# Kernel optimization log

Measured on AMD Instinct MI355X. Metric: run time of the kernel, lower is better.

## Reference

```python
import jax, jax.numpy as jnp
import numpy as np

# ---- static config (from MACEConfig / MACELayerConfig) ----
N_NODES = 128
F_S = 128          # n_invariant_feat_hidden (0e channels)
F_V = 64           # n_vectors_hidden (1e channels)
N_BESSEL = 8       # bessel_number
R_MAX = 5.0        # r_max
N_LAYERS = 2       # n_interactions
HID_RAD = 64       # radial MLP hidden width
F_S_OUT = 128      # n_invariant_feat_readout
F_V_OUT = 64       # n_vectors_readout
AVG_NEIGH = float(N_NODES)  # avg_num_neighbors default = n_nodes
RAD_OUT = F_S + 3 * F_V     # per-edge radial channel weights for the 4 TP paths


def _senders_receivers(n):
    # fully connected graph, matching get_senders_and_receivers
    s = np.repeat(np.arange(n), n - 1)
    j = np.tile(np.arange(1, n), n)
    r = (s + j) % n
    return jnp.asarray(s, dtype=jnp.int32), jnp.asarray(r, dtype=jnp.int32)


def _bessel(r):
    # e3nn bessel basis: sqrt(2/c) sin(n pi r / c) / r, n = 1..N_BESSEL
    n = jnp.arange(1, N_BESSEL + 1, dtype=r.dtype)
    return jnp.sqrt(2.0 / R_MAX) * jnp.sin(n * jnp.pi * r[:, None] / R_MAX) / r[:, None]


def _envelope(r):
    # smooth radial cutoff (polynomial p=6), stand-in for e3nn soft_envelope
    u = r / R_MAX
    p = 6.0
    env = 1.0 - (p + 1) * (p + 2) / 2 * u ** p + p * (p + 2) * u ** (p + 1) - p * (p + 1) / 2 * u ** (p + 2)
    return jnp.where(u < 1.0, env, 0.0)


def _forward(x, species_embed, Wr1, Wr2, W_sv, W_mix_s, W_mix_v, W_out_s, W_out_v):
    senders, receivers = _senders_receivers(N_NODES)

    def single(pos):  # pos: (N, 3)
        com = pos.mean(axis=0)                       # centre of mass (3,)
        v = pos[receivers] - pos[senders]            # edge relative vectors (E, 3)
        r = jnp.linalg.norm(v, axis=-1) + 1e-8       # (E,)
        vhat = v / r[:, None]
        rb = _bessel(r) * _envelope(r)[:, None]      # (E, N_BESSEL)

        s = jnp.broadcast_to(species_embed[0], (N_NODES, F_S))       # 0e node feats
        V = jnp.zeros((N_NODES, F_V, 3), dtype=pos.dtype)            # 1e node feats

        for l in range(N_LAYERS):
            # learned per-edge radial weights for each tensor-product path
            h = jax.nn.silu(rb @ Wr1[l]) @ Wr2[l]    # (E, RAD_OUT)
            R0 = h[:, :F_S]
            R1 = h[:, F_S:F_S + F_V]
            R2 = h[:, F_S + F_V:F_S + 2 * F_V]
            R3 = h[:, F_S + 2 * F_V:]

            s_src = s[senders]                       # gather (E, F_S)
            V_src = V[senders]                       # gather (E, F_V, 3)

            # CG tensor-product paths (only 0e and 1e irreps present):
            m0a = R0 * s_src                                         # 0e x 0e -> 0e
            m0b = R1 * jnp.einsum('efk,ek->ef', V_src, vhat)         # 1e x 1e -> 0e
            m1a = (R2 * (s_src @ W_sv[l]))[..., None] * vhat[:, None, :]  # 0e x 1e -> 1e
            m1b = R3[..., None] * V_src                              # 1e x 0e -> 1e

            # scatter-sum message passing over receivers
            agg0 = jax.ops.segment_sum(jnp.concatenate([m0a, m0b], -1), receivers,
                                       num_segments=N_NODES) / AVG_NEIGH   # (N, F_S+F_V)
            agg1 = jax.ops.segment_sum(jnp.concatenate([m1a, m1b], 1), receivers,
                                       num_segments=N_NODES) / AVG_NEIGH   # (N, 2F_V, 3)

            s = s + jax.nn.silu(agg0 @ W_mix_s[l])
            V = V + jnp.einsum('nfk,fg->ngk', agg1, W_mix_v[l])

        out_s = s @ W_out_s                                          # (N, F_S_OUT)
        out_v = jnp.einsum('nfk,fg->ngk', V, W_out_v) + com          # (N, F_V_OUT, 3) + CoM
        return out_v, out_s

    return jax.vmap(single)(x)


def setup_inputs() -> dict:
    key = jax.random.key(0)
    ks = jax.random.split(key, 10)
    sc = lambda fan: 1.0 / np.sqrt(fan)
    inp = {
        'x': jax.random.normal(ks[0], (8, N_NODES, 3), dtype=jnp.float32),
        'species_embed': jax.random.normal(ks[1], (1, F_S), dtype=jnp.float32),
        'Wr1': jax.random.normal(ks[2], (N_LAYERS, N_BESSEL, HID_RAD), dtype=jnp.float32) * sc(N_BESSEL),
        'Wr2': jax.random.normal(ks[3], (N_LAYERS, HID_RAD, RAD_OUT), dtype=jnp.float32) * sc(HID_RAD),
        'W_sv': jax.random.normal(ks[4], (N_LAYERS, F_S, F_V), dtype=jnp.float32) * sc(F_S),
        'W_mix_s': jax.random.normal(ks[5], (N_LAYERS, F_S + F_V, F_S), dtype=jnp.float32) * sc(F_S + F_V),
        'W_mix_v': jax.random.normal(ks[6], (N_LAYERS, 2 * F_V, F_V), dtype=jnp.float32) * sc(2 * F_V),
        'W_out_s': jax.random.normal(ks[7], (F_S, F_S_OUT), dtype=jnp.float32) * sc(F_S),
        'W_out_v': jax.random.normal(ks[8], (F_V, F_V_OUT), dtype=jnp.float32) * sc(F_V),
    }
    return inp


def reference(x, species_embed, Wr1, Wr2, W_sv, W_mix_s, W_mix_v, W_out_s, W_out_v):
    return _forward(x, species_embed, Wr1, Wr2, W_sv, W_mix_s, W_mix_v, W_out_s, W_out_v)
```

## Files before the change

kernel.cpp:

```cpp
#include <hip/hip_runtime.h>
#include <math.h>

typedef unsigned short u16;
typedef __attribute__((ext_vector_type(8))) short frag_ab;
typedef __attribute__((ext_vector_type(4))) float frag_cd;

#define BATCH 8
#define NN 128
#define FS 128
#define FV 64
#define NB 8
#define HID 64
#define ROUT 320
#define HSTRB 72

#define SZ_S (BATCH*FS*NN)
#define SZ_V (BATCH*FV*3*NN)
#define SZ_T (BATCH*FV*NN)
#define N_W2B (ROUT*HID)
#define OFF_SB 0
#define OFF_VB (OFF_SB+SZ_S)
#define OFF_T1 (OFF_VB+SZ_V)
#define OFF_W2B (OFF_T1+SZ_T)

__device__ __forceinline__ float silu_f(float x){ return x * (1.0f/(1.0f + __expf(-x))); }

__device__ __forceinline__ u16 f2bf(float x){
  union { float f; unsigned int u; } v; v.f = x;
  unsigned int r = v.u + 0x7fffu + ((v.u >> 16) & 1u);
  return (u16)(r >> 16);
}
__device__ __forceinline__ float bf2f(u16 h){
  union { unsigned int u; float f; } v; v.u = ((unsigned int)h) << 16; return v.f;
}

__global__ __launch_bounds__(512) void layer0_kernel(
    const float* __restrict__ pos,
    const float* __restrict__ species,
    const float* __restrict__ Wr1l,
    const float* __restrict__ Wr2,
    const float* __restrict__ Wsv,
    const float* __restrict__ WmixSl,
    const float* __restrict__ WmixVl,
    float* __restrict__ sOut,
    float* __restrict__ vOut,
    float* __restrict__ tOut,
    u16*   __restrict__ w2b)
{
  const int tid = threadIdx.x;
  const int b   = blockIdx.x >> 6;
  const int k0  = (blockIdx.x & 63) * 2;

  __shared__ u16   hidB[2][128*HSTRB];
  __shared__ float vhx[2][128], vhy[2][128], vhz[2][128];
  __shared__ float colsum[2][4][64];
  __shared__ float aggS[2][128];
  __shared__ float dV[2][204];
  __shared__ float sNew[2][128];
  __shared__ float t0L[64];
  __shared__ float tPart[4][2][64];

  const float* pb   = pos + b*NN*3;
  const float* Wr2l = Wr2;

  {
    const int kk   = tid >> 8;
    const int r2   = tid & 255;
    const int i    = r2 & 127;
    const int half = r2 >> 7;
    const int k    = k0 + kk;
    float vx = pb[k*3+0]-pb[i*3+0];
    float vy = pb[k*3+1]-pb[i*3+1];
    float vz = pb[k*3+2]-pb[i*3+2];
    float r = sqrtf(vx*vx+vy*vy+vz*vz) + 1e-8f;
    float inv = 1.0f/r;
    if (half==0){ vhx[kk][i]=vx*inv; vhy[kk][i]=vy*inv; vhz[kk][i]=vz*inv; }
    float u = r*0.2f;
    float env = 0.0f;
    if (u < 1.0f && i != k){
      float u2=u*u, u6=u2*u2*u2;
      env = 1.0f - 28.0f*u6 + 48.0f*u6*u - 21.0f*u6*u2;
    }
    float coef = 0.6324555320336759f * inv * env;
    float th   = r * 0.6283185307179586f;
    float s1 = __sinf(th), c1 = __cosf(th);
    float rb[NB];
    rb[0] = coef*s1;
    float twoc = 2.f*c1, sp = s1, spp = 0.f;
    #pragma unroll
    for(int n=1;n<NB;n++){ float s = twoc*sp - spp; spp = sp; sp = s; rb[n] = coef*s; }
    u16* hrow = hidB[kk] + i*HSTRB;
    #pragma unroll
    for(int jg=0;jg<8;jg++){
      const int jgg = half*8 + jg;
      float h0=0.f,h1=0.f,h2=0.f,h3=0.f;
      #pragma unroll
      for(int n=0;n<NB;n++){
        const float* wr = Wr1l + n*HID + jgg*4;
        float rn = rb[n];
        h0 = fmaf(rn, wr[0], h0);
        h1 = fmaf(rn, wr[1], h1);
        h2 = fmaf(rn, wr[2], h2);
        h3 = fmaf(rn, wr[3], h3);
      }
      ushort4 uu = make_ushort4(f2bf(silu_f(h0)), f2bf(silu_f(h1)),
                                f2bf(silu_f(h2)), f2bf(silu_f(h3)));
      *(ushort4*)(hrow + jgg*4) = uu;
    }
  }
  __syncthreads();

  if (tid < 256){
    const int kk = tid >> 7;
    const int var = (tid >> 5) & 3;
    const int jh  = tid & 31;
    const u16* hb = hidB[kk] + 2*jh;
    float a0=0.f,a1=0.f,c0_=0.f,c1_=0.f;
    if (var == 0){
      #pragma unroll 8
      for (int i=0;i<128;i+=2){
        unsigned int v0 = *(const unsigned int*)(hb + i*HSTRB);
        unsigned int v1 = *(const unsigned int*)(hb + (i+1)*HSTRB);
        a0  += bf2f((u16)(v0 & 0xffffu)); a1  += bf2f((u16)(v0 >> 16));
        c0_ += bf2f((u16)(v1 & 0xffffu)); c1_ += bf2f((u16)(v1 >> 16));
      }
    } else {
      const float* wv = (var==1) ? vhx[kk] : (var==2) ? vhy[kk] : vhz[kk];
      #pragma unroll 8
      for (int i=0;i<128;i+=2){
        unsigned int v0 = *(const unsigned int*)(hb + i*HSTRB);
        unsigned int v1 = *(const unsigned int*)(hb + (i+1)*HSTRB);
        float w0 = wv[i], w1 = wv[i+1];
        a0  = fmaf(bf2f((u16)(v0 & 0xffffu)), w0, a0);
        a1  = fmaf(bf2f((u16)(v0 >> 16)),     w0, a1);
        c0_ = fmaf(bf2f((u16)(v1 & 0xffffu)), w1, c0_);
        c1_ = fmaf(bf2f((u16)(v1 >> 16)),     w1, c1_);
      }
    }
    colsum[kk][var][2*jh]   = a0+c0_;
    colsum[kk][var][2*jh+1] = a1+c1_;
  }
  __syncthreads();

  if (tid < 128){
    const int c = tid;
    float d0=0.f, d1=0.f;
    #pragma unroll 2
    for (int j0=0;j0<HID;j0+=4){
      float4 s0 = *(const float4*)&colsum[0][0][j0];
      float4 s1 = *(const float4*)&colsum[1][0][j0];
      float w0 = Wr2l[j0*ROUT + c];
      float w1 = Wr2l[(j0+1)*ROUT + c];
      float w2 = Wr2l[(j0+2)*ROUT + c];
      float w3 = Wr2l[(j0+3)*ROUT + c];
      d0 = fmaf(s0.x,w0,d0); d0 = fmaf(s0.y,w1,d0); d0 = fmaf(s0.z,w2,d0); d0 = fmaf(s0.w,w3,d0);
      d1 = fmaf(s1.x,w0,d1); d1 = fmaf(s1.y,w1,d1); d1 = fmaf(s1.z,w2,d1); d1 = fmaf(s1.w,w3,d1);
    }
    float sc = species[c] * (1.0f/128.0f);
    aggS[0][c] = sc * d0;
    aggS[1][c] = sc * d1;
  } else if (tid < 320){
    const int o = tid - 128;
    const int f = o & 63, c3 = o >> 6;
    float d0=0.f, d1=0.f;
    #pragma unroll 2
    for (int j0=0;j0<HID;j0+=4){
      float4 s0 = *(const float4*)&colsum[0][1+c3][j0];
      float4 s1 = *(const float4*)&colsum[1][1+c3][j0];
      float w0 = Wr2l[j0*ROUT + 192 + f];
      float w1 = Wr2l[(j0+1)*ROUT + 192 + f];
      float w2 = Wr2l[(j0+2)*ROUT + 192 + f];
      float w3 = Wr2l[(j0+3)*ROUT + 192 + f];
      d0 = fmaf(s0.x,w0,d0); d0 = fmaf(s0.y,w1,d0); d0 = fmaf(s0.z,w2,d0); d0 = fmaf(s0.w,w3,d0);
      d1 = fmaf(s1.x,w0,d1); d1 = fmaf(s1.y,w1,d1); d1 = fmaf(s1.z,w2,d1); d1 = fmaf(s1.w,w3,d1);
    }
    dV[0][c3*68+f] = d0 * (1.0f/128.0f);
    dV[1][c3*68+f] = d1 * (1.0f/128.0f);
  } else if (tid < 384){
    const int g = tid - 320;
    float a0=0.f, a1=0.f;
    #pragma unroll 8
    for (int c=0; c<FS; c+=2){
      a0 = fmaf(species[c],   Wsv[c*FV+g],     a0);
      a1 = fmaf(species[c+1], Wsv[(c+1)*FV+g], a1);
    }
    t0L[g] = a0+a1;
  } else if (tid < 424){
    const int t = blockIdx.x*40 + (tid-384);
    const int j = t & 63, c = t >> 6;
    w2b[t] = f2bf(Wr2[HID*ROUT + j*ROUT + c]);
  }
  __syncthreads();

  if (tid < FS){
    float a0=0.f, a1=0.f;
    #pragma unroll 2
    for (int c0=0; c0<128; c0+=4){
      float4 g0 = *(const float4*)&aggS[0][c0];
      float4 g1 = *(const float4*)&aggS[1][c0];
      float w0 = WmixSl[c0*FS+tid];
      float w1 = WmixSl[(c0+1)*FS+tid];
      float w2 = WmixSl[(c0+2)*FS+tid];
      float w3 = WmixSl[(c0+3)*FS+tid];
      a0 = fmaf(g0.x,w0,a0); a0 = fmaf(g0.y,w1,a0); a0 = fmaf(g0.z,w2,a0); a0 = fmaf(g0.w,w3,a0);
      a1 = fmaf(g1.x,w0,a1); a1 = fmaf(g1.y,w1,a1); a1 = fmaf(g1.z,w2,a1); a1 = fmaf(g1.w,w3,a1);
    }
    float sn0 = species[tid] + silu_f(a0);
    float sn1 = species[tid] + silu_f(a1);
    sNew[0][tid] = sn0;
    sNew[1][tid] = sn1;
    sOut[(b*FS+tid)*NN + k0]     = sn0;
    sOut[(b*FS+tid)*NN + k0 + 1] = sn1;
  } else if (tid < 320){
    const int o = tid - 128;
    const int g = o/3, c3 = o - g*3;
    float a0=0.f, a1=0.f;
    #pragma unroll 2
    for (int f0=0; f0<FV; f0+=4){
      float4 dv0 = *(const float4*)&dV[0][c3*68+f0];
      float4 dv1 = *(const float4*)&dV[1][c3*68+f0];
      float4 t4  = *(const float4*)&t0L[f0];
      float w0 = WmixVl[f0*FV+g];
      float w1 = WmixVl[(f0+1)*FV+g];
      float w2 = WmixVl[(f0+2)*FV+g];
      float w3 = WmixVl[(f0+3)*FV+g];
      a0 = fmaf(t4.x*dv0.x, w0, a0); a0 = fmaf(t4.y*dv0.y, w1, a0);
      a0 = fmaf(t4.z*dv0.z, w2, a0); a0 = fmaf(t4.w*dv0.w, w3, a0);
      a1 = fmaf(t4.x*dv1.x, w0, a1); a1 = fmaf(t4.y*dv1.y, w1, a1);
      a1 = fmaf(t4.z*dv1.z, w2, a1); a1 = fmaf(t4.w*dv1.w, w3, a1);
    }
    vOut[(b*FV*3 + o)*NN + k0]     = a0;
    vOut[(b*FV*3 + o)*NN + k0 + 1] = a1;
  }
  __syncthreads();

  if (tid < 256){
    const int g = tid & 63, p = tid >> 6;
    const float* Wsv1 = Wsv + FS*FV;
    const int f0 = p*32;
    float a0=0.f, a1=0.f;
    #pragma unroll 2
    for (int f=f0; f<f0+32; f+=4){
      float4 s0 = *(const float4*)&sNew[0][f];
      float4 s1 = *(const float4*)&sNew[1][f];
      float w0 = Wsv1[f*FV+g];
      float w1 = Wsv1[(f+1)*FV+g];
      float w2 = Wsv1[(f+2)*FV+g];
      float w3 = Wsv1[(f+3)*FV+g];
      a0 = fmaf(s0.x,w0,a0); a0 = fmaf(s0.y,w1,a0); a0 = fmaf(s0.z,w2,a0); a0 = fmaf(s0.w,w3,a0);
      a1 = fmaf(s1.x,w0,a1); a1 = fmaf(s1.y,w1,a1); a1 = fmaf(s1.z,w2,a1); a1 = fmaf(s1.w,w3,a1);
    }
    tPart[p][0][g] = a0; tPart[p][1][g] = a1;
  }
  __syncthreads();
  if (tid < 128){
    const int g = tid & 63, kk = tid >> 6;
    tOut[(b*FV+g)*NN + k0 + kk] =
        tPart[0][kk][g] + tPart[1][kk][g] + tPart[2][kk][g] + tPart[3][kk][g];
  }
}

__global__ __launch_bounds__(512, 2) void layer_kernel(
    const float* __restrict__ pos,
    const float* __restrict__ sIn,
    const float* __restrict__ vIn,
    const float* __restrict__ tIn,
    const float* __restrict__ Wr1l,
    const u16*   __restrict__ w2bl,
    const float* __restrict__ WmixSl,
    const float* __restrict__ WmixVl,
    const float* __restrict__ WoutS,
    const float* __restrict__ WoutV,
    float* __restrict__ outp)
{
  const int tid  = threadIdx.x;
  const int b    = blockIdx.x >> 5;
  const int k0   = (blockIdx.x & 31) * 4;
  const int w    = tid >> 6;
  const int lane = tid & 63;
  const int col  = lane & 15;
  const int quad = lane >> 4;
  const int wq   = w & 3;
  const int sh   = w >> 2;

  __shared__ u16   hidB[4][128*HSTRB];
  __shared__ float vhx[4][128], vhy[4][128], vhz[4][128];
  __shared__ float aggP[4][2][600];
  __shared__ float sPart[4][2][FS];
  __shared__ float sNew[4][FS];
  __shared__ float vNewL[4][204];
  __shared__ float comL[3];

  const float* pb = pos + b*NN*3;

  {
    const int kk = tid >> 7;
    const int i  = tid & 127;
    const int k  = k0 + kk;
    float vx = pb[k*3+0]-pb[i*3+0];
    float vy = pb[k*3+1]-pb[i*3+1];
    float vz = pb[k*3+2]-pb[i*3+2];
    float r = sqrtf(vx*vx+vy*vy+vz*vz) + 1e-8f;
    float inv = 1.0f/r;
    vhx[kk][i]=vx*inv; vhy[kk][i]=vy*inv; vhz[kk][i]=vz*inv;
    float u = r*0.2f;
    float env = 0.0f;
    if (u < 1.0f && i != k){
      float u2=u*u, u6=u2*u2*u2;
      env = 1.0f - 28.0f*u6 + 48.0f*u6*u - 21.0f*u6*u2;
    }
    float coef = 0.6324555320336759f * inv * env;
    float th   = r * 0.6283185307179586f;
    float s1 = __sinf(th), c1 = __cosf(th);
    float rb[NB];
    rb[0] = coef*s1;
    float twoc = 2.f*c1, sp = s1, spp = 0.f;
    #pragma unroll
    for(int n=1;n<NB;n++){ float s = twoc*sp - spp; spp = sp; sp = s; rb[n] = coef*s; }
    u16* hrow = hidB[kk] + i*HSTRB;
    #pragma unroll
    for(int jg=0;jg<16;jg++){
      float h0=0.f,h1=0.f,h2=0.f,h3=0.f;
      #pragma unroll
      for(int n=0;n<NB;n++){
        const float* wr = Wr1l + n*HID + jg*4;
        float rn = rb[n];
        h0 = fmaf(rn, wr[0], h0);
        h1 = fmaf(rn, wr[1], h1);
        h2 = fmaf(rn, wr[2], h2);
        h3 = fmaf(rn, wr[3], h3);
      }
      ushort4 uu = make_ushort4(f2bf(silu_f(h0)), f2bf(silu_f(h1)),
                                f2bf(silu_f(h2)), f2bf(silu_f(h3)));
      *(ushort4*)(hrow + jg*4) = uu;
    }
    if (tid < 3){
      float a0=0.f, a1=0.f;
      for (int n=0;n<NN;n+=2){ a0 += pb[n*3+tid]; a1 += pb[(n+1)*3+tid]; }
      comL[tid] = (a0+a1) * (1.0f/128.0f);
    }
  }
  __syncthreads();

  const float* sIb = sIn + b*FS*NN;
  const float* vIb = vIn + b*FV*3*NN;
  const float* tIb = tIn + b*FV*NN;
  const int i00 = sh*64 + quad*4;

  {
    const int c_s0 = wq*16 + col;
    const int c_s1 = 64 + c_s0;
    const int f_vc = c_s0;

    const u16* wp0 = w2bl + c_s0*HID + quad*8;
    const u16* wp1 = w2bl + c_s1*HID + quad*8;
    const u16* wp2 = w2bl + (128 + f_vc)*HID + quad*8;
    const u16* wp3 = w2bl + (192 + f_vc)*HID + quad*8;
    const u16* wp4 = w2bl + (256 + f_vc)*HID + quad*8;
    const frag_ab b00 = *(const frag_ab*)(wp0), b01 = *(const frag_ab*)(wp0+32);
    const frag_ab b10 = *(const frag_ab*)(wp1), b11 = *(const frag_ab*)(wp1+32);
    const frag_ab b20 = *(const frag_ab*)(wp2), b21 = *(const frag_ab*)(wp2+32);
    const frag_ab b30 = *(const frag_ab*)(wp3), b31 = *(const frag_ab*)(wp3+32);
    const frag_ab b40 = *(const frag_ab*)(wp4), b41 = *(const frag_ab*)(wp4+32);

    const float* fs0 = sIb + c_s0*NN + i00;
    const float* fs1 = sIb + c_s1*NN + i00;
    const float* fv  = vIb + f_vc*3*NN + i00;
    const float* ft  = tIb + f_vc*NN + i00;

    float sA0[4]={0.f,0.f,0.f,0.f}, sA1[4]={0.f,0.f,0.f,0.f}, sA2[4]={0.f,0.f,0.f,0.f};
    float sX3[4]={0.f,0.f,0.f,0.f}, sY3[4]={0.f,0.f,0.f,0.f}, sZ3[4]={0.f,0.f,0.f,0.f};
    float sX4[4]={0.f,0.f,0.f,0.f}, sY4[4]={0.f,0.f,0.f,0.f}, sZ4[4]={0.f,0.f,0.f,0.f};

    #pragma unroll 1
    for (int mt=0; mt<4; mt++){
      float4 s4a = *(const float4*)&fs0[mt*16];
      float4 s4b = *(const float4*)&fs1[mt*16];
      float4 vx4 = *(const float4*)&fv[mt*16];
      float4 vy4 = *(const float4*)&fv[NN + mt*16];
      float4 vz4 = *(const float4*)&fv[2*NN + mt*16];
      float4 t4  = *(const float4*)&ft[mt*16];
      const int hbase = (sh*64 + mt*16 + col)*HSTRB + quad*8;
      const int vbase = i00 + mt*16;
      #pragma unroll
      for (int kk=0; kk<4; kk++){
        frag_ab a0 = *(const frag_ab*)&hidB[kk][hbase];
        frag_ab a1 = *(const frag_ab*)&hidB[kk][hbase + 32];
        float4 hx4 = *(const float4*)&vhx[kk][vbase];
        float4 hy4 = *(const float4*)&vhy[kk][vbase];
        float4 hz4 = *(const float4*)&vhz[kk][vbase];
        frag_cd ac0 = {0.f,0.f,0.f,0.f};
        frag_cd ac1 = {0.f,0.f,0.f,0.f};
        frag_cd ac2 = {0.f,0.f,0.f,0.f};
        frag_cd ac3 = {0.f,0.f,0.f,0.f};
        frag_cd ac4 = {0.f,0.f,0.f,0.f};
        ac0 = __builtin_amdgcn_mfma_f32_16x16x32_bf16(a0, b00, ac0, 0,0,0);
        ac1 = __builtin_amdgcn_mfma_f32_16x16x32_bf16(a0, b10, ac1, 0,0,0);
        ac2 = __builtin_amdgcn_mfma_f32_16x16x32_bf16(a0, b20, ac2, 0,0,0);
        ac3 = __builtin_amdgcn_mfma_f32_16x16x32_bf16(a0, b30, ac3, 0,0,0);
        ac4 = __builtin_amdgcn_mfma_f32_16x16x32_bf16(a0, b40, ac4, 0,0,0);
        ac0 = __builtin_amdgcn_mfma_f32_16x16x32_bf16(a1, b01, ac0, 0,0,0);
        ac1 = __builtin_amdgcn_mfma_f32_16x16x32_bf16(a1, b11, ac1, 0,0,0);
        ac2 = __builtin_amdgcn_mfma_f32_16x16x32_bf16(a1, b21, ac2, 0,0,0);
        ac3 = __builtin_amdgcn_mfma_f32_16x16x32_bf16(a1, b31, ac3, 0,0,0);
        ac4 = __builtin_amdgcn_mfma_f32_16x16x32_bf16(a1, b41, ac4, 0,0,0);

        sA0[kk] += ac0[0]*s4a.x + ac0[1]*s4a.y + ac0[2]*s4a.z + ac0[3]*s4a.w;
        sA1[kk] += ac1[0]*s4b.x + ac1[1]*s4b.y + ac1[2]*s4b.z + ac1[3]*s4b.w;
        sA2[kk] += ac2[0]*(vx4.x*hx4.x + vy4.x*hy4.x + vz4.x*hz4.x)
                 + ac2[1]*(vx4.y*hx4.y + vy4.y*hy4.y + vz4.y*hz4.y)
                 + ac2[2]*(vx4.z*hx4.z + vy4.z*hy4.z + vz4.z*hz4.z)
                 + ac2[3]*(vx4.w*hx4.w + vy4.w*hy4.w + vz4.w*hz4.w);
        float t0_ = ac3[0]*t4.x, t1_ = ac3[1]*t4.y, t2_ = ac3[2]*t4.z, t3_ = ac3[3]*t4.w;
        sX3[kk] += t0_*hx4.x + t1_*hx4.y + t2_*hx4.z + t3_*hx4.w;
        sY3[kk] += t0_*hy4.x + t1_*hy4.y + t2_*hy4.z + t3_*hy4.w;
        sZ3[kk] += t0_*hz4.x + t1_*hz4.y + t2_*hz4.z + t3_*hz4.w;
        sX4[kk] += ac4[0]*vx4.x + ac4[1]*vx4.y + ac4[2]*vx4.z + ac4[3]*vx4.w;
        sY4[kk] += ac4[0]*vy4.x + ac4[1]*vy4.y + ac4[2]*vy4.z + ac4[3]*vy4.w;
        sZ4[kk] += ac4[0]*vz4.x + ac4[1]*vz4.y + ac4[2]*vz4.z + ac4[3]*vz4.w;
      }
    }

    #pragma unroll
    for (int kk=0; kk<4; kk++){
      float v0 = sA0[kk]; v0 += __shfl_xor(v0,16,64); v0 += __shfl_xor(v0,32,64);
      float v1 = sA1[kk]; v1 += __shfl_xor(v1,16,64); v1 += __shfl_xor(v1,32,64);
      float v2 = sA2[kk]; v2 += __shfl_xor(v2,16,64); v2 += __shfl_xor(v2,32,64);
      float x3 = sX3[kk]; x3 += __shfl_xor(x3,16,64); x3 += __shfl_xor(x3,32,64);
      float y3 = sY3[kk]; y3 += __shfl_xor(y3,16,64); y3 += __shfl_xor(y3,32,64);
      float z3 = sZ3[kk]; z3 += __shfl_xor(z3,16,64); z3 += __shfl_xor(z3,32,64);
      float x4 = sX4[kk]; x4 += __shfl_xor(x4,16,64); x4 += __shfl_xor(x4,32,64);
      float y4 = sY4[kk]; y4 += __shfl_xor(y4,16,64); y4 += __shfl_xor(y4,32,64);
      float z4 = sZ4[kk]; z4 += __shfl_xor(z4,16,64); z4 += __shfl_xor(z4,32,64);
      if (lane < 16){
        aggP[kk][sh][wq*16 + lane]        = v0;
        aggP[kk][sh][64 + wq*16 + lane]   = v1;
        aggP[kk][sh][128 + wq*16 + lane]  = v2;
        const int f2 = wq*16 + lane;
        aggP[kk][sh][192       + f2] = x3;
        aggP[kk][sh][192 +  68 + f2] = y3;
        aggP[kk][sh][192 + 136 + f2] = z3;
        aggP[kk][sh][396       + f2] = x4;
        aggP[kk][sh][396 +  68 + f2] = y4;
        aggP[kk][sh][396 + 136 + f2] = z4;
      }
    }
  }

  __syncthreads();
  for (int t2=tid; t2<2400; t2+=512){
    const int kk = t2 / 600;
    const int t  = t2 - kk*600;
    aggP[kk][0][t] = (aggP[kk][0][t] + aggP[kk][1][t]) * (1.0f/128.0f);
  }
  __syncthreads();

  if (tid < 256){
    const int o = tid & 127, p = tid >> 7;
    const int c0 = p*96;
    float a0=0.f,a1=0.f,a2=0.f,a3=0.f;
    #pragma unroll 2
    for (int cc=c0; cc<c0+96; cc+=4){
      float4 g0 = *(const float4*)&aggP[0][0][cc];
      float4 g1 = *(const float4*)&aggP[1][0][cc];
      float4 g2 = *(const float4*)&aggP[2][0][cc];
      float4 g3 = *(const float4*)&aggP[3][0][cc];
      float w0 = WmixSl[cc*FS+o];
      float w1 = WmixSl[(cc+1)*FS+o];
      float w2 = WmixSl[(cc+2)*FS+o];
      float w3 = WmixSl[(cc+3)*FS+o];
      a0 = fmaf(g0.x,w0,a0); a0 = fmaf(g0.y,w1,a0); a0 = fmaf(g0.z,w2,a0); a0 = fmaf(g0.w,w3,a0);
      a1 = fmaf(g1.x,w0,a1); a1 = fmaf(g1.y,w1,a1); a1 = fmaf(g1.z,w2,a1); a1 = fmaf(g1.w,w3,a1);
      a2 = fmaf(g2.x,w0,a2); a2 = fmaf(g2.y,w1,a2); a2 = fmaf(g2.z,w2,a2); a2 = fmaf(g2.w,w3,a2);
      a3 = fmaf(g3.x,w0,a3); a3 = fmaf(g3.y,w1,a3); a3 = fmaf(g3.z,w2,a3); a3 = fmaf(g3.w,w3,a3);
    }
    sPart[0][p][o] = a0; sPart[1][p][o] = a1;
    sPart[2][p][o] = a2; sPart[3][p][o] = a3;
  } else if (tid < 448){
    const int o = tid - 256;
    const int c3 = o >> 6, g = o & 63;
    float a0=0.f,a1=0.f,a2=0.f,a3=0.f;
    #pragma unroll 1
    for (int f0=0; f0<FV; f0+=4){
      float4 p0 = *(const float4*)&aggP[0][0][192+c3*68+f0];
      float4 q0 = *(const float4*)&aggP[0][0][396+c3*68+f0];
      float4 p1 = *(const float4*)&aggP[1][0][192+c3*68+f0];
      float4 q1 = *(const float4*)&aggP[1][0][396+c3*68+f0];
      float4 p2 = *(const float4*)&aggP[2][0][192+c3*68+f0];
      float4 q2 = *(const float4*)&aggP[2][0][396+c3*68+f0];
      float4 p3 = *(const float4*)&aggP[3][0][192+c3*68+f0];
      float4 q3 = *(const float4*)&aggP[3][0][396+c3*68+f0];
      float w00 = WmixVl[f0*FV+g];
      float w01 = WmixVl[(f0+1)*FV+g];
      float w02 = WmixVl[(f0+2)*FV+g];
      float w03 = WmixVl[(f0+3)*FV+g];
      float w10 = WmixVl[(f0+FV)*FV+g];
      float w11 = WmixVl[(f0+FV+1)*FV+g];
      float w12 = WmixVl[(f0+FV+2)*FV+g];
      float w13 = WmixVl[(f0+FV+3)*FV+g];
      a0 = fmaf(p0.x,w00,a0); a0 = fmaf(p0.y,w01,a0); a0 = fmaf(p0.z,w02,a0); a0 = fmaf(p0.w,w03,a0);
      a0 = fmaf(q0.x,w10,a0); a0 = fmaf(q0.y,w11,a0); a0 = fmaf(q0.z,w12,a0); a0 = fmaf(q0.w,w13,a0);
      a1 = fmaf(p1.x,w00,a1); a1 = fmaf(p1.y,w01,a1); a1 = fmaf(p1.z,w02,a1); a1 = fmaf(p1.w,w03,a1);
      a1 = fmaf(q1.x,w10,a1); a1 = fmaf(q1.y,w11,a1); a1 = fmaf(q1.z,w12,a1); a1 = fmaf(q1.w,w13,a1);
      a2 = fmaf(p2.x,w00,a2); a2 = fmaf(p2.y,w01,a2); a2 = fmaf(p2.z,w02,a2); a2 = fmaf(p2.w,w03,a2);
      a2 = fmaf(q2.x,w10,a2); a2 = fmaf(q2.y,w11,a2); a2 = fmaf(q2.z,w12,a2); a2 = fmaf(q2.w,w13,a2);
      a3 = fmaf(p3.x,w00,a3); a3 = fmaf(p3.y,w01,a3); a3 = fmaf(p3.z,w02,a3); a3 = fmaf(p3.w,w03,a3);
      a3 = fmaf(q3.x,w10,a3); a3 = fmaf(q3.y,w11,a3); a3 = fmaf(q3.z,w12,a3); a3 = fmaf(q3.w,w13,a3);
    }
    const int oo = g*3 + c3;
    vNewL[0][c3*68+g] = vIb[oo*NN + k0]     + a0;
    vNewL[1][c3*68+g] = vIb[oo*NN + k0 + 1] + a1;
    vNewL[2][c3*68+g] = vIb[oo*NN + k0 + 2] + a2;
    vNewL[3][c3*68+g] = vIb[oo*NN + k0 + 3] + a3;
  }
  __syncthreads();

  if (tid < FS){
    #pragma unroll
    for (int kk=0; kk<4; kk++)
      sNew[kk][tid] = sIb[tid*NN + k0 + kk]
                    + silu_f(sPart[kk][0][tid] + sPart[kk][1][tid]);
  } else if (tid < 320){
    const int o = tid - 128;
    const int g = o/3, c3 = o - g*3;
    float a0 = comL[c3], a1 = comL[c3], a2 = comL[c3], a3 = comL[c3];
    #pragma unroll 2
    for (int f0=0; f0<FV; f0+=4){
      float4 v0 = *(const float4*)&vNewL[0][c3*68+f0];
      float4 v1 = *(const float4*)&vNewL[1][c3*68+f0];
      float4 v2 = *(const float4*)&vNewL[2][c3*68+f0];
      float4 v3 = *(const float4*)&vNewL[3][c3*68+f0];
      float w0 = WoutV[f0*FV+g];
      float w1 = WoutV[(f0+1)*FV+g];
      float w2 = WoutV[(f0+2)*FV+g];
      float w3 = WoutV[(f0+3)*FV+g];
      a0 = fmaf(v0.x,w0,a0); a0 = fmaf(v0.y,w1,a0); a0 = fmaf(v0.z,w2,a0); a0 = fmaf(v0.w,w3,a0);
      a1 = fmaf(v1.x,w0,a1); a1 = fmaf(v1.y,w1,a1); a1 = fmaf(v1.z,w2,a1); a1 = fmaf(v1.w,w3,a1);
      a2 = fmaf(v2.x,w0,a2); a2 = fmaf(v2.y,w1,a2); a2 = fmaf(v2.z,w2,a2); a2 = fmaf(v2.w,w3,a2);
      a3 = fmaf(v3.x,w0,a3); a3 = fmaf(v3.y,w1,a3); a3 = fmaf(v3.z,w2,a3); a3 = fmaf(v3.w,w3,a3);
    }
    outp[(b*NN+k0)*FV*3 + o]   = a0;
    outp[(b*NN+k0+1)*FV*3 + o] = a1;
    outp[(b*NN+k0+2)*FV*3 + o] = a2;
    outp[(b*NN+k0+3)*FV*3 + o] = a3;
  }
  __syncthreads();

  float* e3s = &aggP[0][0][0];
  if (tid < 512){
    const int o = tid & 127, p = tid >> 7;
    const int f0 = p*32;
    float a0=0.f,a1=0.f,a2=0.f,a3=0.f;
    #pragma unroll 2
    for (int f=f0; f<f0+32; f+=4){
      float4 s0 = *(const float4*)&sNew[0][f];
      float4 s1 = *(const float4*)&sNew[1][f];
      float4 s2 = *(const float4*)&sNew[2][f];
      float4 s3 = *(const float4*)&sNew[3][f];
      float w0 = WoutS[f*FS+o];
      float w1 = WoutS[(f+1)*FS+o];
      float w2 = WoutS[(f+2)*FS+o];
      float w3 = WoutS[(f+3)*FS+o];
      a0 = fmaf(s0.x,w0,a0); a0 = fmaf(s0.y,w1,a0); a0 = fmaf(s0.z,w2,a0); a0 = fmaf(s0.w,w3,a0);
      a1 = fmaf(s1.x,w0,a1); a1 = fmaf(s1.y,w1,a1); a1 = fmaf(s1.z,w2,a1); a1 = fmaf(s1.w,w3,a1);
      a2 = fmaf(s2.x,w0,a2); a2 = fmaf(s2.y,w1,a2); a2 = fmaf(s2.z,w2,a2); a2 = fmaf(s2.w,w3,a2);
      a3 = fmaf(s3.x,w0,a3); a3 = fmaf(s3.y,w1,a3); a3 = fmaf(s3.z,w2,a3); a3 = fmaf(s3.w,w3,a3);
    }
    e3s[(p*4+0)*128 + o] = a0;
    e3s[(p*4+1)*128 + o] = a1;
    e3s[(p*4+2)*128 + o] = a2;
    e3s[(p*4+3)*128 + o] = a3;
  }
  __syncthreads();

  if (tid < 512){
    const int o = tid & 127, kk = tid >> 7;
    float a = e3s[(0*4+kk)*128 + o] + e3s[(1*4+kk)*128 + o]
            + e3s[(2*4+kk)*128 + o] + e3s[(3*4+kk)*128 + o];
    outp[BATCH*NN*FV*3 + (b*NN+k0+kk)*FS + o] = a;
  }
}

extern "C" void kernel_launch(void* const* d_in, const int* in_sizes, int n_in,
                              void* d_out, int out_size, void* d_ws, size_t ws_size,
                              hipStream_t stream)
{
  const float* x       = (const float*)d_in[0];
  const float* species = (const float*)d_in[1];
  const float* Wr1     = (const float*)d_in[2];
  const float* Wr2     = (const float*)d_in[3];
  const float* Wsv     = (const float*)d_in[4];
  const float* WmixS   = (const float*)d_in[5];
  const float* WmixV   = (const float*)d_in[6];
  const float* WoutS   = (const float*)d_in[7];
  const float* WoutV   = (const float*)d_in[8];
  float* ws  = (float*)d_ws;
  float* out = (float*)d_out;

  float* sB  = ws + OFF_SB;
  float* vB  = ws + OFF_VB;
  float* t1  = ws + OFF_T1;
  u16*   w2b = (u16*)(ws + OFF_W2B);

  layer0_kernel<<<BATCH*NN/2, 512, 0, stream>>>(x, species, Wr1, Wr2, Wsv,
      WmixS, WmixV, sB, vB, t1, w2b);

  layer_kernel<<<BATCH*NN/4, 512, 0, stream>>>(x, sB, vB, t1,
      Wr1 + NB*HID, w2b, WmixS + 192*FS, WmixV + 128*FV,
      WoutS, WoutV, out);
}
```

Measured before the change: 127.1 us.

## Process four receiver nodes per block in layer0 kernel instead of two

The layer0 kernel now handles four receiver nodes per block, halving the grid to 256 blocks. Each thread computes one edge's full 64-wide hidden row instead of half. Weight loads from Wr2, WmixS, WmixV and Wsv are reused across four nodes rather than two, and the w2b conversion slice per block doubles to 80. The cost is double the shared memory (about 80KB), fewer blocks to fill the GPU, and more registers per thread, with launch bounds set to 2 blocks per CU.

```diff
diff --git a/kernel.cpp b/kernel.cpp
--- a/kernel.cpp
+++ b/kernel.cpp
@@ -34,7 +34,7 @@
   union { unsigned int u; float f; } v; v.u = ((unsigned int)h) << 16; return v.f;
 }
 
-__global__ __launch_bounds__(512) void layer0_kernel(
+__global__ __launch_bounds__(512, 2) void layer0_kernel(
     const float* __restrict__ pos,
     const float* __restrict__ species,
     const float* __restrict__ Wr1l,
@@ -48,33 +48,31 @@
     u16*   __restrict__ w2b)
 {
   const int tid = threadIdx.x;
-  const int b   = blockIdx.x >> 6;
-  const int k0  = (blockIdx.x & 63) * 2;
-
-  __shared__ u16   hidB[2][128*HSTRB];
-  __shared__ float vhx[2][128], vhy[2][128], vhz[2][128];
-  __shared__ float colsum[2][4][64];
-  __shared__ float aggS[2][128];
-  __shared__ float dV[2][204];
-  __shared__ float sNew[2][128];
+  const int b   = blockIdx.x >> 5;
+  const int k0  = (blockIdx.x & 31) * 4;
+
+  __shared__ u16   hidB[4][128*HSTRB];
+  __shared__ float vhx[4][128], vhy[4][128], vhz[4][128];
+  __shared__ float colsum[4][4][64];
+  __shared__ float aggS[4][128];
+  __shared__ float dV[4][204];
+  __shared__ float sNew[4][128];
   __shared__ float t0L[64];
-  __shared__ float tPart[4][2][64];
+  __shared__ float tPart[4][4][64];
 
   const float* pb   = pos + b*NN*3;
   const float* Wr2l = Wr2;
 
   {
-    const int kk   = tid >> 8;
-    const int r2   = tid & 255;
-    const int i    = r2 & 127;
-    const int half = r2 >> 7;
-    const int k    = k0 + kk;
+    const int kk = tid >> 7;
+    const int i  = tid & 127;
+    const int k  = k0 + kk;
     float vx = pb[k*3+0]-pb[i*3+0];
     float vy = pb[k*3+1]-pb[i*3+1];
     float vz = pb[k*3+2]-pb[i*3+2];
     float r = sqrtf(vx*vx+vy*vy+vz*vz) + 1e-8f;
     float inv = 1.0f/r;
-    if (half==0){ vhx[kk][i]=vx*inv; vhy[kk][i]=vy*inv; vhz[kk][i]=vz*inv; }
+    vhx[kk][i]=vx*inv; vhy[kk][i]=vy*inv; vhz[kk][i]=vz*inv;
     float u = r*0.2f;
     float env = 0.0f;
     if (u < 1.0f && i != k){
@@ -91,12 +89,11 @@
     for(int n=1;n<NB;n++){ float s = twoc*sp - spp; spp = sp; sp = s; rb[n] = coef*s; }
     u16* hrow = hidB[kk] + i*HSTRB;
     #pragma unroll
-    for(int jg=0;jg<8;jg++){
-      const int jgg = half*8 + jg;
+    for(int jg=0;jg<16;jg++){
       float h0=0.f,h1=0.f,h2=0.f,h3=0.f;
       #pragma unroll
       for(int n=0;n<NB;n++){
-        const float* wr = Wr1l + n*HID + jgg*4;
+        const float* wr = Wr1l + n*HID + jg*4;
         float rn = rb[n];
         h0 = fmaf(rn, wr[0], h0);
         h1 = fmaf(rn, wr[1], h1);
@@ -105,13 +102,13 @@
       }
       ushort4 uu = make_ushort4(f2bf(silu_f(h0)), f2bf(silu_f(h1)),
                                 f2bf(silu_f(h2)), f2bf(silu_f(h3)));
-      *(ushort4*)(hrow + jgg*4) = uu;
-    }
-  }
-  __syncthreads();
-
-  if (tid < 256){
-    const int kk = tid >> 7;
+      *(ushort4*)(hrow + jg*4) = uu;
+    }
+  }
+  __syncthreads();
+
+  {
+    const int kk  = tid >> 7;
     const int var = (tid >> 5) & 3;
     const int jh  = tid & 31;
     const u16* hb = hidB[kk] + 2*jh;
@@ -144,38 +141,50 @@
 
   if (tid < 128){
     const int c = tid;
-    float d0=0.f, d1=0.f;
+    float d0=0.f, d1=0.f, d2=0.f, d3=0.f;
     #pragma unroll 2
     for (int j0=0;j0<HID;j0+=4){
       float4 s0 = *(const float4*)&colsum[0][0][j0];
       float4 s1 = *(const float4*)&colsum[1][0][j0];
+      float4 s2 = *(const float4*)&colsum[2][0][j0];
+      float4 s3 = *(const float4*)&colsum[3][0][j0];
       float w0 = Wr2l[j0*ROUT + c];
       float w1 = Wr2l[(j0+1)*ROUT + c];
       float w2 = Wr2l[(j0+2)*ROUT + c];
       float w3 = Wr2l[(j0+3)*ROUT + c];
       d0 = fmaf(s0.x,w0,d0); d0 = fmaf(s0.y,w1,d0); d0 = fmaf(s0.z,w2,d0); d0 = fmaf(s0.w,w3,d0);
       d1 = fmaf(s1.x,w0,d1); d1 = fmaf(s1.y,w1,d1); d1 = fmaf(s1.z,w2,d1); d1 = fmaf(s1.w,w3,d1);
+      d2 = fmaf(s2.x,w0,d2); d2 = fmaf(s2.y,w1,d2); d2 = fmaf(s2.z,w2,d2); d2 = fmaf(s2.w,w3,d2);
+      d3 = fmaf(s3.x,w0,d3); d3 = fmaf(s3.y,w1,d3); d3 = fmaf(s3.z,w2,d3); d3 = fmaf(s3.w,w3,d3);
     }
     float sc = species[c] * (1.0f/128.0f);
     aggS[0][c] = sc * d0;
     aggS[1][c] = sc * d1;
+    aggS[2][c] = sc * d2;
+    aggS[3][c] = sc * d3;
   } else if (tid < 320){
     const int o = tid - 128;
     const int f = o & 63, c3 = o >> 6;
-    float d0=0.f, d1=0.f;
+    float d0=0.f, d1=0.f, d2=0.f, d3=0.f;
     #pragma unroll 2
     for (int j0=0;j0<HID;j0+=4){
       float4 s0 = *(const float4*)&colsum[0][1+c3][j0];
       float4 s1 = *(const float4*)&colsum[1][1+c3][j0];
+      float4 s2 = *(const float4*)&colsum[2][1+c3][j0];
+      float4 s3 = *(const float4*)&colsum[3][1+c3][j0];
       float w0 = Wr2l[j0*ROUT + 192 + f];
       float w1 = Wr2l[(j0+1)*ROUT + 192 + f];
       float w2 = Wr2l[(j0+2)*ROUT + 192 + f];
       float w3 = Wr2l[(j0+3)*ROUT + 192 + f];
       d0 = fmaf(s0.x,w0,d0); d0 = fmaf(s0.y,w1,d0); d0 = fmaf(s0.z,w2,d0); d0 = fmaf(s0.w,w3,d0);
       d1 = fmaf(s1.x,w0,d1); d1 = fmaf(s1.y,w1,d1); d1 = fmaf(s1.z,w2,d1); d1 = fmaf(s1.w,w3,d1);
+      d2 = fmaf(s2.x,w0,d2); d2 = fmaf(s2.y,w1,d2); d2 = fmaf(s2.z,w2,d2); d2 = fmaf(s2.w,w3,d2);
+      d3 = fmaf(s3.x,w0,d3); d3 = fmaf(s3.y,w1,d3); d3 = fmaf(s3.z,w2,d3); d3 = fmaf(s3.w,w3,d3);
     }
     dV[0][c3*68+f] = d0 * (1.0f/128.0f);
     dV[1][c3*68+f] = d1 * (1.0f/128.0f);
+    dV[2][c3*68+f] = d2 * (1.0f/128.0f);
+    dV[3][c3*68+f] = d3 * (1.0f/128.0f);
   } else if (tid < 384){
     const int g = tid - 320;
     float a0=0.f, a1=0.f;
@@ -185,52 +194,69 @@
       a1 = fmaf(species[c+1], Wsv[(c+1)*FV+g], a1);
     }
     t0L[g] = a0+a1;
-  } else if (tid < 424){
-    const int t = blockIdx.x*40 + (tid-384);
+  } else if (tid < 464){
+    const int t = blockIdx.x*80 + (tid-384);
     const int j = t & 63, c = t >> 6;
     w2b[t] = f2bf(Wr2[HID*ROUT + j*ROUT + c]);
   }
   __syncthreads();
 
   if (tid < FS){
-    float a0=0.f, a1=0.f;
+    float a0=0.f, a1=0.f, a2=0.f, a3=0.f;
     #pragma unroll 2
     for (int c0=0; c0<128; c0+=4){
       float4 g0 = *(const float4*)&aggS[0][c0];
       float4 g1 = *(const float4*)&aggS[1][c0];
+      float4 g2 = *(const float4*)&aggS[2][c0];
+      float4 g3 = *(const float4*)&aggS[3][c0];
       float w0 = WmixSl[c0*FS+tid];
       float w1 = WmixSl[(c0+1)*FS+tid];
       float w2 = WmixSl[(c0+2)*FS+tid];
       float w3 = WmixSl[(c0+3)*FS+tid];
       a0 = fmaf(g0.x,w0,a0); a0 = fmaf(g0.y,w1,a0); a0 = fmaf(g0.z,w2,a0); a0 = fmaf(g0.w,w3,a0);
       a1 = fmaf(g1.x,w0,a1); a1 = fmaf(g1.y,w1,a1); a1 = fmaf(g1.z,w2,a1); a1 = fmaf(g1.w,w3,a1);
+      a2 = fmaf(g2.x,w0,a2); a2 = fmaf(g2.y,w1,a2); a2 = fmaf(g2.z,w2,a2); a2 = fmaf(g2.w,w3,a2);
+      a3 = fmaf(g3.x,w0,a3); a3 = fmaf(g3.y,w1,a3); a3 = fmaf(g3.z,w2,a3); a3 = fmaf(g3.w,w3,a3);
     }
     float sn0 = species[tid] + silu_f(a0);
     float sn1 = species[tid] + silu_f(a1);
-    sNew[0][tid] = sn0;
-    sNew[1][tid] = sn1;
+    float sn2 = species[tid] + silu_f(a2);
+    float sn3 = species[tid] + silu_f(a3);
+    sNew[0][tid] = sn0; sNew[1][tid] = sn1;
+    sNew[2][tid] = sn2; sNew[3][tid] = sn3;
     sOut[(b*FS+tid)*NN + k0]     = sn0;
     sOut[(b*FS+tid)*NN + k0 + 1] = sn1;
+    sOut[(b*FS+tid)*NN + k0 + 2] = sn2;
+    sOut[(b*FS+tid)*NN + k0 + 3] = sn3;
   } else if (tid < 320){
     const int o = tid - 128;
     const int g = o/3, c3 = o - g*3;
-    float a0=0.f, a1=0.f;
+    float a0=0.f, a1=0.f, a2=0.f, a3=0.f;
     #pragma unroll 2
     for (int f0=0; f0<FV; f0+=4){
       float4 dv0 = *(const float4*)&dV[0][c3*68+f0];
       float4 dv1 = *(const float4*)&dV[1][c3*68+f0];
+      float4 dv2 = *(const float4*)&dV[2][c3*68+f0];
+      float4 dv3 = *(const float4*)&dV[3][c3*68+f0];
       float4 t4  = *(const float4*)&t0L[f0];
       float w0 = WmixVl[f0*FV+g];
       float w1 = WmixVl[(f0+1)*FV+g];
       float w2 = WmixVl[(f0+2)*FV+g];
       float w3 = WmixVl[(f0+3)*FV+g];
-      a0 = fmaf(t4.x*dv0.x, w0, a0); a0 = fmaf(t4.y*dv0.y, w1, a0);
-      a0 = fmaf(t4.z*dv0.z, w2, a0); a0 = fmaf(t4.w*dv0.w, w3, a0);
-      a1 = fmaf(t4.x*dv1.x, w0, a1); a1 = fmaf(t4.y*dv1.y, w1, a1);
-      a1 = fmaf(t4.z*dv1.z, w2, a1); a1 = fmaf(t4.w*dv1.w, w3, a1);
+      float tw0 = t4.x*w0, tw1 = t4.y*w1, tw2 = t4.z*w2, tw3 = t4.w*w3;
+      a0 = fmaf(dv0.x, tw0, a0); a0 = fmaf(dv0.y, tw1, a0);
+      a0 = fmaf(dv0.z, tw2, a0); a0 = fmaf(dv0.w, tw3, a0);
+      a1 = fmaf(dv1.x, tw0, a1); a1 = fmaf(dv1.y, tw1, a1);
+      a1 = fmaf(dv1.z, tw2, a1); a1 = fmaf(dv1.w, tw3, a1);
+      a2 = fmaf(dv2.x, tw0, a2); a2 = fmaf(dv2.y, tw1, a2);
+      a2 = fmaf(dv2.z, tw2, a2); a2 = fmaf(dv2.w, tw3, a2);
+      a3 = fmaf(dv3.x, tw0, a3); a3 = fmaf(dv3.y, tw1, a3);
+      a3 = fmaf(dv3.z, tw2, a3); a3 = fmaf(dv3.w, tw3, a3);
     }
     vOut[(b*FV*3 + o)*NN + k0]     = a0;
     vOut[(b*FV*3 + o)*NN + k0 + 1] = a1;
+    vOut[(b*FV*3 + o)*NN + k0 + 2] = a2;
+    vOut[(b*FV*3 + o)*NN + k0 + 3] = a3;
   }
   __syncthreads();
 
@@ -238,22 +264,27 @@
     const int g = tid & 63, p = tid >> 6;
     const float* Wsv1 = Wsv + FS*FV;
     const int f0 = p*32;
-    float a0=0.f, a1=0.f;
+    float a0=0.f, a1=0.f, a2=0.f, a3=0.f;
     #pragma unroll 2
     for (int f=f0; f<f0+32; f+=4){
       float4 s0 = *(const float4*)&sNew[0][f];
       float4 s1 = *(const float4*)&sNew[1][f];
+      float4 s2 = *(const float4*)&sNew[2][f];
+      float4 s3 = *(const float4*)&sNew[3][f];
       float w0 = Wsv1[f*FV+g];
       float w1 = Wsv1[(f+1)*FV+g];
       float w2 = Wsv1[(f+2)*FV+g];
       float w3 = Wsv1[(f+3)*FV+g];
       a0 = fmaf(s0.x,w0,a0); a0 = fmaf(s0.y,w1,a0); a0 = fmaf(s0.z,w2,a0); a0 = fmaf(s0.w,w3,a0);
       a1 = fmaf(s1.x,w0,a1); a1 = fmaf(s1.y,w1,a1); a1 = fmaf(s1.z,w2,a1); a1 = fmaf(s1.w,w3,a1);
+      a2 = fmaf(s2.x,w0,a2); a2 = fmaf(s2.y,w1,a2); a2 = fmaf(s2.z,w2,a2); a2 = fmaf(s2.w,w3,a2);
+      a3 = fmaf(s3.x,w0,a3); a3 = fmaf(s3.y,w1,a3); a3 = fmaf(s3.z,w2,a3); a3 = fmaf(s3.w,w3,a3);
     }
     tPart[p][0][g] = a0; tPart[p][1][g] = a1;
-  }
-  __syncthreads();
-  if (tid < 128){
+    tPart[p][2][g] = a2; tPart[p][3][g] = a3;
+  }
+  __syncthreads();
+  if (tid < 256){
     const int g = tid & 63, kk = tid >> 6;
     tOut[(b*FV+g)*NN + k0 + kk] =
         tPart[0][kk][g] + tPart[1][kk][g] + tPart[2][kk][g] + tPart[3][kk][g];
@@ -602,7 +633,7 @@
   float* t1  = ws + OFF_T1;
   u16*   w2b = (u16*)(ws + OFF_W2B);
 
-  layer0_kernel<<<BATCH*NN/2, 512, 0, stream>>>(x, species, Wr1, Wr2, Wsv,
+  layer0_kernel<<<BATCH*NN/4, 512, 0, stream>>>(x, species, Wr1, Wr2, Wsv,
       WmixS, WmixV, sB, vB, t1, w2b);
 
   layer_kernel<<<BATCH*NN/4, 512, 0, stream>>>(x, sB, vB, t1,
```

Result: no change. 129.2 us (+1.7%).
